# Kernel optimization log

Hardware: AMD Instinct MI355X
Metric: run time of the kernel (lower is better)

Reference implementation:

```python
import jax, jax.numpy as jnp
import numpy as np

ALPHA = 0.2  # leakyrelu negative slope
NEG_INF = -1.0e12


def setup_inputs() -> dict:
    key = jax.random.key(0)
    k1, k2, k3, k4, k5 = jax.random.split(key, 5)
    B, N, C_in, C_out = 8, 2048, 256, 256
    inp = jax.random.normal(k1, (B, N, C_in), dtype=jnp.float32)
    adj = jax.random.randint(k2, (N, N), 0, 2, dtype=jnp.int32)
    # xavier_uniform with gain=1.414 for (C_in, C_out)
    limit = 1.414 * np.sqrt(6.0 / (C_in + C_out))
    W1 = jax.random.uniform(k3, (C_in, C_out), jnp.float32, -limit, limit)
    W2 = jax.random.uniform(k4, (C_in, C_out), jnp.float32, -limit, limit)
    W3 = jax.random.uniform(k5, (C_in, C_out), jnp.float32, -limit, limit)
    return {"inp": inp, "adj": adj, "W1": W1, "W2": W2, "W3": W3}


def reference(inp, adj, W1, W2, W3):
    # inp: [B,N,Cin], adj: [N,N], W*: [Cin,Cout]
    h1 = jnp.einsum('bnc,cd->bnd', inp, W1)  # [B,N,Cout] queries
    h2 = jnp.einsum('bnc,cd->bnd', inp, W2)  # [B,N,Cout] keys
    h3 = jnp.einsum('bnc,cd->bnd', inp, W3)  # [B,N,Cout] values
    e = jnp.einsum('bnd,bmd->bnm', h1, h2)   # [B,N,N] scores
    e = jax.nn.leaky_relu(e, ALPHA)
    e = jnp.where(adj[None, :, :] > 0, e, NEG_INF)
    attention = jax.nn.softmax(e, axis=-1)   # dropout p=0 / eval mode -> identity
    h_prime = jnp.einsum('bnm,bmd->bnd', attention, h3)
    return jax.nn.relu(h_prime)  # concat=True
```

## Files before the change

### kernel.cpp

```cpp
#include <hip/hip_runtime.h>

typedef __bf16 bf16_t;
typedef __bf16 bf16x4 __attribute__((ext_vector_type(4)));
typedef __bf16 bf16x8 __attribute__((ext_vector_type(8)));
typedef float floatx4 __attribute__((ext_vector_type(4)));
typedef signed char i8_t;
typedef int intx4 __attribute__((ext_vector_type(4)));

__device__ inline void split_hl(float v, bf16_t& hi, bf16_t& lo) {
    hi = (bf16_t)v;
    lo = (bf16_t)(v - (float)hi);
}

__global__ void wtrans_kernel(const float* __restrict__ W1,
                              const float* __restrict__ W2,
                              const float* __restrict__ W3,
                              bf16_t* __restrict__ Wthi, bf16_t* __restrict__ Wtlo) {
    __shared__ float T[64 * 68];
    const int zi = blockIdx.z;
    const float* W = (zi == 0) ? W1 : ((zi == 1) ? W2 : W3);
    bf16_t* ohi = Wthi + zi * 256 * 256;
    bf16_t* olo = Wtlo + zi * 256 * 256;
    const int c0 = blockIdx.x * 64, d0 = blockIdx.y * 64;
    const int tid = threadIdx.x;
#pragma unroll
    for (int i = 0; i < 4; i++) {
        int idx = i * 256 + tid;
        int r = idx >> 4, c4 = (idx & 15) * 4;
        floatx4 v = *(const floatx4*)(W + (c0 + r) * 256 + d0 + c4);
        *(floatx4*)(&T[r * 68 + c4]) = v;
    }
    __syncthreads();
#pragma unroll
    for (int i = 0; i < 4; i++) {
        int idx = i * 256 + tid;
        int rd = idx & 63, cc4 = (idx >> 6) * 4;
        bf16x4 vh, vl;
#pragma unroll
        for (int ii = 0; ii < 4; ii++) {
            float v = T[(cc4 + ii) * 68 + rd];
            bf16_t h, l; split_hl(v, h, l);
            vh[ii] = h; vl[ii] = l;
        }
        *(bf16x4*)(ohi + (d0 + rd) * 256 + c0 + cc4) = vh;
        *(bf16x4*)(olo + (d0 + rd) * 256 + c0 + cc4) = vl;
    }
}

__global__ __launch_bounds__(256) void projadj_kernel(
    const float* __restrict__ X,
    const bf16_t* __restrict__ Wthi, const bf16_t* __restrict__ Wtlo,
    i8_t* __restrict__ Q8h, i8_t* __restrict__ Q8l, float* __restrict__ sqv,
    i8_t* __restrict__ K8h, i8_t* __restrict__ K8l, float* __restrict__ skv,
    bf16_t* __restrict__ H3t,
    const int* __restrict__ adj, unsigned* __restrict__ bits) {
    __shared__ __align__(16) char SM[51712];
    bf16_t* Xh = (bf16_t*)(SM);
    bf16_t* Xl = (bf16_t*)(SM + 5120);
    bf16_t* Wh = (bf16_t*)(SM + 10240);
    bf16_t* Wl = (bf16_t*)(SM + 30720);
    float* amS = (float*)(SM + 51200);

    const int tid = threadIdx.x;
    const int blk = blockIdx.x;
    if (blk < 512) {
        int id = blk * 256 + tid;
        const int* p = adj + (size_t)id * 32;
        unsigned wbits = 0;
#pragma unroll
        for (int j = 0; j < 32; j += 4) {
            int4 v = *(const int4*)(p + j);
            wbits |= (v.x > 0 ? 1u : 0u) << j;
            wbits |= (v.y > 0 ? 1u : 0u) << (j + 1);
            wbits |= (v.z > 0 ? 1u : 0u) << (j + 2);
            wbits |= (v.w > 0 ? 1u : 0u) << (j + 3);
        }
        bits[id] = wbits;
        return;
    }

    const int pblk = blk - 512;
    const int z = pblk >> 8;
    const int row0 = (pblk & 255) * 64;
    const int w = tid >> 6, lane = tid & 63;
    const int m = lane & 15, q = lane >> 4;
    const int wr = w >> 1, wc = w & 1;
    const bf16_t* Wzh = Wthi + z * 256 * 256;
    const bf16_t* Wzl = Wtlo + z * 256 * 256;

    floatx4 acc[16];
#pragma unroll
    for (int i = 0; i < 16; i++) acc[i] = (floatx4){0.f, 0.f, 0.f, 0.f};

    for (int c0 = 0; c0 < 256; c0 += 32) {
#pragma unroll
        for (int i = 0; i < 2; i++) {
            int idx = i * 256 + tid;
            int r = idx >> 3, c4 = (idx & 7) * 4;
            floatx4 v = *(const floatx4*)(X + (size_t)(row0 + r) * 256 + c0 + c4);
            bf16x4 vh, vl;
#pragma unroll
            for (int ii = 0; ii < 4; ii++) {
                bf16_t h, l; split_hl(v[ii], h, l);
                vh[ii] = h; vl[ii] = l;
            }
            *(bf16x4*)(&Xh[r * 40 + c4]) = vh;
            *(bf16x4*)(&Xl[r * 40 + c4]) = vl;
        }
#pragma unroll
        for (int i = 0; i < 4; i++) {
            int idx = i * 256 + tid;
            int d = idx >> 2, c8 = (idx & 3) * 8;
            *(bf16x8*)(&Wh[d * 40 + c8]) = *(const bf16x8*)(Wzh + d * 256 + c0 + c8);
            *(bf16x8*)(&Wl[d * 40 + c8]) = *(const bf16x8*)(Wzl + d * 256 + c0 + c8);
        }
        __syncthreads();
        bf16x8 ah[2], al[2];
#pragma unroll
        for (int rt = 0; rt < 2; rt++) {
            ah[rt] = *(const bf16x8*)(&Xh[(wr * 32 + rt * 16 + m) * 40 + q * 8]);
            al[rt] = *(const bf16x8*)(&Xl[(wr * 32 + rt * 16 + m) * 40 + q * 8]);
        }
#pragma unroll
        for (int ct = 0; ct < 8; ct++) {
            bf16x8 bh = *(const bf16x8*)(&Wh[(wc * 128 + ct * 16 + m) * 40 + q * 8]);
            bf16x8 bl = *(const bf16x8*)(&Wl[(wc * 128 + ct * 16 + m) * 40 + q * 8]);
#pragma unroll
            for (int rt = 0; rt < 2; rt++) {
                acc[rt * 8 + ct] = __builtin_amdgcn_mfma_f32_16x16x32_bf16(ah[rt], bh, acc[rt * 8 + ct], 0, 0, 0);
                acc[rt * 8 + ct] = __builtin_amdgcn_mfma_f32_16x16x32_bf16(ah[rt], bl, acc[rt * 8 + ct], 0, 0, 0);
                acc[rt * 8 + ct] = __builtin_amdgcn_mfma_f32_16x16x32_bf16(al[rt], bh, acc[rt * 8 + ct], 0, 0, 0);
            }
        }
        __syncthreads();
    }

    if (z < 2) {
        i8_t* Dh = (z == 0) ? Q8h : K8h;
        i8_t* Dl = (z == 0) ? Q8l : K8l;
        float* sv = (z == 0) ? sqv : skv;
        float am[2][4];
#pragma unroll
        for (int rt = 0; rt < 2; rt++)
#pragma unroll
            for (int r = 0; r < 4; r++) am[rt][r] = 0.f;
#pragma unroll
        for (int ct = 0; ct < 8; ct++)
#pragma unroll
            for (int rt = 0; rt < 2; rt++)
#pragma unroll
                for (int r = 0; r < 4; r++)
                    am[rt][r] = fmaxf(am[rt][r], fabsf(acc[rt * 8 + ct][r]));
#pragma unroll
        for (int off = 1; off < 16; off <<= 1)
#pragma unroll
            for (int rt = 0; rt < 2; rt++)
#pragma unroll
                for (int r = 0; r < 4; r++)
                    am[rt][r] = fmaxf(am[rt][r], __shfl_xor(am[rt][r], off, 64));
        if (m == 0) {
#pragma unroll
            for (int rt = 0; rt < 2; rt++)
#pragma unroll
                for (int r = 0; r < 4; r++)
                    amS[wc * 64 + wr * 32 + rt * 16 + q * 4 + r] = am[rt][r];
        }
        __syncthreads();
        float sc[2][4], inv[2][4];
#pragma unroll
        for (int rt = 0; rt < 2; rt++)
#pragma unroll
            for (int r = 0; r < 4; r++) {
                int row = wr * 32 + rt * 16 + q * 4 + r;
                float a = fmaxf(amS[row], amS[64 + row]);
                sc[rt][r]  = (a > 0.f) ? a * (1.f / 127.f) : 1.f;
                inv[rt][r] = (a > 0.f) ? 127.f / a : 0.f;
            }
#pragma unroll
        for (int ct = 0; ct < 8; ct++)
#pragma unroll
            for (int rt = 0; rt < 2; rt++)
#pragma unroll
                for (int r = 0; r < 4; r++) {
                    float vq = acc[rt * 8 + ct][r] * inv[rt][r];
                    float qh = rintf(vq);
                    float ql = fminf(fmaxf(rintf((vq - qh) * 256.f), -127.f), 127.f);
                    int offo = (row0 + wr * 32 + rt * 16 + q * 4 + r) * 256 +
                               wc * 128 + ct * 16 + m;
                    Dh[offo] = (i8_t)(int)qh;
                    Dl[offo] = (i8_t)(int)ql;
                }
        if (m == 0 && wc == 0) {
#pragma unroll
            for (int rt = 0; rt < 2; rt++)
#pragma unroll
                for (int r = 0; r < 4; r++)
                    sv[row0 + wr * 32 + rt * 16 + q * 4 + r] = sc[rt][r];
        }
    } else {
        char* VtB = SM;
#pragma unroll
        for (int ct = 0; ct < 8; ct++)
#pragma unroll
            for (int rt = 0; rt < 2; rt++) {
                int d = wc * 128 + ct * 16 + m;
                int n0 = wr * 32 + rt * 16 + q * 4;
                bf16x4 v4;
#pragma unroll
                for (int r = 0; r < 4; r++) v4[r] = (bf16_t)acc[rt * 8 + ct][r];
                *(bf16x4*)(VtB + d * 136 + n0 * 2) = v4;
            }
        __syncthreads();
        const int bb = row0 >> 11;
        const int nbase = row0 & 2047;
        bf16_t* Hrow = H3t + (size_t)bb * 256 * 2048 + nbase;
#pragma unroll
        for (int it = 0; it < 16; it++) {
            int d = it * 16 + (tid >> 4);
            int c8 = tid & 15;
            bf16x4 v = *(const bf16x4*)(VtB + d * 136 + c8 * 8);
            *(bf16x4*)(Hrow + (size_t)d * 2048 + c8 * 4) = v;
        }
    }
}

#define K8SW(row, off) ((off) ^ (((row) & 7) << 4))
#define VSW(row, off)  ((off) ^ ((((row) >> 1) & 3) << 4))
__global__ __launch_bounds__(256, 2) void attn_kernel(
    const i8_t* __restrict__ Q8h, const i8_t* __restrict__ Q8l,
    const float* __restrict__ sqv,
    const i8_t* __restrict__ K8h, const i8_t* __restrict__ K8l,
    const float* __restrict__ skv,
    const bf16_t* __restrict__ H3t, const unsigned* __restrict__ adjbits,
    bf16_t* __restrict__ Opart, float* __restrict__ mpart, float* __restrict__ lpart,
    int klen) {
    __shared__ i8_t K8[2][2][32 * 256];
    __shared__ bf16_t Vl[2][256 * 32];
    __shared__ bf16_t Pl[4][16 * 32];

    const int nwg = (int)(gridDim.x * gridDim.y * gridDim.z);
    const int wgid = (int)(blockIdx.x + (blockIdx.y << 5) + (blockIdx.z << 8));
    const int nid = (wgid & 7) * (nwg >> 3) + (wgid >> 3);
    const int qb = nid & 31;
    const int b  = (nid >> 5) & 7;
    const int kz = nid >> 8;

    const int q0 = qb * 64;
    const int tid = threadIdx.x;
    const int w = tid >> 6, lane = tid & 63;
    const int m = lane & 15, q = lane >> 4;

    char* PlB = (char*)&Pl[w][0];

    const i8_t* qrh = Q8h + (size_t)(b * 2048 + q0 + w * 16 + m) * 256;
    const i8_t* qrl = Q8l + (size_t)(b * 2048 + q0 + w * 16 + m) * 256;
    intx4 qh8[4], ql8[4];
#pragma unroll
    for (int ck = 0; ck < 4; ck++) {
        qh8[ck] = *(const intx4*)(qrh + ck * 64 + q * 16);
        ql8[ck] = *(const intx4*)(qrl + ck * 64 + q * 16);
    }
    float sq4[4];
#pragma unroll
    for (int r = 0; r < 4; r++) sq4[r] = sqv[b * 2048 + q0 + w * 16 + q * 4 + r];

    bf16x8 vones;
#pragma unroll
    for (int i = 0; i < 8; i++) vones[i] = (bf16_t)1.0f;

    float m_run[4];
#pragma unroll
    for (int r = 0; r < 4; r++) m_run[r] = -3.0e38f;
    floatx4 l_acc = (floatx4){0.f, 0.f, 0.f, 0.f};
    floatx4 o[16];
#pragma unroll
    for (int i = 0; i < 16; i++) o[i] = (floatx4){0.f, 0.f, 0.f, 0.f};

    const unsigned* bitrow[4];
#pragma unroll
    for (int r = 0; r < 4; r++)
        bitrow[r] = adjbits + (size_t)(q0 + w * 16 + q * 4 + r) * 64;

    intx4 rkh[2], rkl[2];
    bf16x8 rvv[4];
    float skt[2], skn[2];
    const int kbeg = kz * klen, kend = kbeg + klen;

#pragma unroll
    for (int i = 0; i < 2; i++) {
        int ci = i * 256 + tid;
        int kr = ci >> 4, cb = (ci & 15) * 16;
        rkh[i] = *(const intx4*)(K8h + (size_t)(b * 2048 + kbeg + kr) * 256 + cb);
        rkl[i] = *(const intx4*)(K8l + (size_t)(b * 2048 + kbeg + kr) * 256 + cb);
    }
#pragma unroll
    for (int i = 0; i < 4; i++) {
        int ci = i * 256 + tid;
        int d = ci >> 2, k8 = (ci & 3) * 8;
        rvv[i] = *(const bf16x8*)(H3t + (size_t)(b * 256 + d) * 2048 + kbeg + k8);
    }
    skt[0] = skv[b * 2048 + kbeg + m];
    skt[1] = skv[b * 2048 + kbeg + 16 + m];

    int kbuf = 0;
    for (int k0 = kbeg; k0 < kend; k0 += 32) {
        char* KB0 = (char*)&K8[kbuf][0][0];
        char* KB1 = (char*)&K8[kbuf][1][0];
        char* VB  = (char*)&Vl[kbuf][0];
#pragma unroll
        for (int i = 0; i < 2; i++) {
            int ci = i * 256 + tid;
            int kr = ci >> 4, cb = (ci & 15) * 16;
            *(intx4*)(KB0 + K8SW(kr, kr * 256 + cb)) = rkh[i];
            *(intx4*)(KB1 + K8SW(kr, kr * 256 + cb)) = rkl[i];
        }
#pragma unroll
        for (int i = 0; i < 4; i++) {
            int ci = i * 256 + tid;
            int d = ci >> 2, kb = (ci & 3) * 16;
            *(bf16x8*)(VB + VSW(d, d * 64 + kb)) = rvv[i];
        }
        __syncthreads();

        if (k0 + 32 < kend) {
            int kn = k0 + 32;
#pragma unroll
            for (int i = 0; i < 2; i++) {
                int ci = i * 256 + tid;
                int kr = ci >> 4, cb = (ci & 15) * 16;
                rkh[i] = *(const intx4*)(K8h + (size_t)(b * 2048 + kn + kr) * 256 + cb);
                rkl[i] = *(const intx4*)(K8l + (size_t)(b * 2048 + kn + kr) * 256 + cb);
            }
#pragma unroll
            for (int i = 0; i < 4; i++) {
                int ci = i * 256 + tid;
                int d = ci >> 2, k8 = (ci & 3) * 8;
                rvv[i] = *(const bf16x8*)(H3t + (size_t)(b * 256 + d) * 2048 + kn + k8);
            }
            skn[0] = skv[b * 2048 + kn + m];
            skn[1] = skv[b * 2048 + kn + 16 + m];
        }

        float s[2][4];
#pragma unroll
        for (int t = 0; t < 2; t++) {
            intx4 ch = {0, 0, 0, 0}, cm = {0, 0, 0, 0};
            const int row = t * 16 + m;
#pragma unroll
            for (int ck = 0; ck < 4; ck++) {
                const int cb2 = ck * 64 + q * 16;
                intx4 kh = *(const intx4*)(KB0 + K8SW(row, row * 256 + cb2));
                intx4 kl = *(const intx4*)(KB1 + K8SW(row, row * 256 + cb2));
                ch = __builtin_amdgcn_mfma_i32_16x16x64_i8(qh8[ck], kh, ch, 0, 0, 0);
                cm = __builtin_amdgcn_mfma_i32_16x16x64_i8(qh8[ck], kl, cm, 0, 0, 0);
                cm = __builtin_amdgcn_mfma_i32_16x16x64_i8(ql8[ck], kh, cm, 0, 0, 0);
            }
#pragma unroll
            for (int r = 0; r < 4; r++)
                s[t][r] = fmaf((float)cm[r], 0.00390625f, (float)ch[r]) * (sq4[r] * skt[t]);
        }

        unsigned aw[4];
#pragma unroll
        for (int r = 0; r < 4; r++) aw[r] = bitrow[r][k0 >> 5];
        float p[2][4], tmax[4];
#pragma unroll
        for (int r = 0; r < 4; r++) tmax[r] = -3.0e38f;
#pragma unroll
        for (int t = 0; t < 2; t++)
#pragma unroll
            for (int r = 0; r < 4; r++) {
                float v = s[t][r];
                v = (v > 0.f) ? v : 0.2f * v;
                v = ((aw[r] >> (t * 16 + m)) & 1u) ? v : -1.0e12f;
                p[t][r] = v;
                tmax[r] = fmaxf(tmax[r], v);
            }
#pragma unroll
        for (int off = 1; off < 16; off <<= 1)
#pragma unroll
            for (int r = 0; r < 4; r++)
                tmax[r] = fmaxf(tmax[r], __shfl_xor(tmax[r], off, 64));

        int rise = 0;
#pragma unroll
        for (int r = 0; r < 4; r++)
            rise |= (tmax[r] > m_run[r] + 8.f);
        if (__any(rise)) {
#pragma unroll
            for (int r = 0; r < 4; r++) {
                float mnew = fmaxf(m_run[r], tmax[r]);
                float alpha = __expf(m_run[r] - mnew);
                m_run[r] = mnew;
                l_acc[r] *= alpha;
#pragma unroll
                for (int nt = 0; nt < 16; nt++) o[nt][r] *= alpha;
            }
        }
#pragma unroll
        for (int t = 0; t < 2; t++)
#pragma unroll
            for (int r = 0; r < 4; r++)
                p[t][r] = __expf(p[t][r] - m_run[r]);

#pragma unroll
        for (int t = 0; t < 2; t++)
#pragma unroll
            for (int r = 0; r < 4; r++) {
                int row = q * 4 + r;
                *(bf16_t*)(PlB + VSW(row, row * 64 + (t * 16 + m) * 2)) = (bf16_t)p[t][r];
            }
        bf16x8 pf = *(const bf16x8*)(PlB + VSW(m, m * 64 + q * 16));

        l_acc = __builtin_amdgcn_mfma_f32_16x16x32_bf16(pf, vones, l_acc, 0, 0, 0);

#pragma unroll
        for (int nt = 0; nt < 16; nt++) {
            const int vr = nt * 16 + m;
            bf16x8 vf = *(const bf16x8*)(VB + VSW(vr, vr * 64 + q * 16));
            o[nt] = __builtin_amdgcn_mfma_f32_16x16x32_bf16(pf, vf, o[nt], 0, 0, 0);
        }
        skt[0] = skn[0];
        skt[1] = skn[1];
        kbuf ^= 1;
    }

    const int rowg = kz * 16384 + b * 2048 + q0 + w * 16 + q * 4;
#pragma unroll
    for (int nt = 0; nt < 16; nt++)
#pragma unroll
        for (int r = 0; r < 4; r++)
            Opart[(size_t)(rowg + r) * 256 + nt * 16 + m] = (bf16_t)o[nt][r];
    if (m == 0) {
#pragma unroll
        for (int r = 0; r < 4; r++) {
            mpart[rowg + r] = m_run[r];
            lpart[rowg + r] = l_acc[r];
        }
    }
}

__global__ __launch_bounds__(256) void merge_kernel(
    const bf16_t* __restrict__ Opart, const float* __restrict__ mpart,
    const float* __restrict__ lpart, float* __restrict__ out, int S) {
    int gid = blockIdx.x * 256 + threadIdx.x;
    int row = gid >> 6, c4 = (gid & 63) * 4;
    float M = -3.0e38f;
    for (int s = 0; s < S; s++) M = fmaxf(M, mpart[s * 16384 + row]);
    float denom = 0.f;
    float4 acc = make_float4(0.f, 0.f, 0.f, 0.f);
    for (int s = 0; s < S; s++) {
        float sc = __expf(mpart[s * 16384 + row] - M);
        denom += lpart[s * 16384 + row] * sc;
        bf16x4 v = *(const bf16x4*)(Opart + ((size_t)(s * 16384 + row)) * 256 + c4);
        acc.x += (float)v[0] * sc; acc.y += (float)v[1] * sc;
        acc.z += (float)v[2] * sc; acc.w += (float)v[3] * sc;
    }
    float inv = 1.f / denom;
    float4 r;
    r.x = fmaxf(acc.x * inv, 0.f);
    r.y = fmaxf(acc.y * inv, 0.f);
    r.z = fmaxf(acc.z * inv, 0.f);
    r.w = fmaxf(acc.w * inv, 0.f);
    *(float4*)(out + (size_t)row * 256 + c4) = r;
}

extern "C" void kernel_launch(void* const* d_in, const int* in_sizes, int n_in,
                              void* d_out, int out_size, void* d_ws, size_t ws_size,
                              hipStream_t stream) {
    const float* X   = (const float*)d_in[0];
    const int*   adj = (const int*)d_in[1];
    const float* W1  = (const float*)d_in[2];
    const float* W2  = (const float*)d_in[3];
    const float* W3  = (const float*)d_in[4];
    float* out = (float*)d_out;

    char* ws = (char*)d_ws;
    i8_t* Q8h = (i8_t*)(ws + ((size_t)0 << 20));
    i8_t* Q8l = (i8_t*)(ws + ((size_t)4 << 20));
    i8_t* K8h = (i8_t*)(ws + ((size_t)8 << 20));
    i8_t* K8l = (i8_t*)(ws + ((size_t)12 << 20));
    bf16_t* H3t = (bf16_t*)(ws + ((size_t)16 << 20));
    float* sqv = (float*)(ws + ((size_t)24 << 20));
    float* skv = (float*)(ws + ((size_t)24 << 20) + 65536);
    size_t wt0 = ((size_t)24 << 20) + 131072;
    bf16_t* Wthi = (bf16_t*)(ws + wt0);
    bf16_t* Wtlo = (bf16_t*)(ws + wt0 + 393216);
    float* mpart = (float*)(ws + wt0);
    float* lpart = (float*)(ws + wt0 + 131072);
    unsigned* adjb = (unsigned*)(ws + wt0 + 786432);
    size_t opart_off = wt0 + 786432 + 524288;
    const size_t need2 = opart_off + (size_t)2 * 16384 * 256 * 2;

    int S = (ws_size >= need2) ? 2 : 1;
    bf16_t* Opart = (bf16_t*)(ws + opart_off);

    wtrans_kernel<<<dim3(4, 4, 3), 256, 0, stream>>>(W1, W2, W3, Wthi, Wtlo);
    projadj_kernel<<<1280, 256, 0, stream>>>(X, Wthi, Wtlo,
                                             Q8h, Q8l, sqv, K8h, K8l, skv, H3t,
                                             adj, adjb);
    attn_kernel<<<dim3(32, 8, S), 256, 0, stream>>>(Q8h, Q8l, sqv, K8h, K8l, skv,
                                                    H3t, adjb, Opart, mpart, lpart,
                                                    2048 / S);
    merge_kernel<<<4096, 256, 0, stream>>>(Opart, mpart, lpart, out, S);
}
```

Before: 209.5 us.

## Double-buffer X tiles, read W directly from global, add MFMA priority hints

The projection kernel now register-prefetches the next X chunk and double-buffers the X shared tiles, which removes the trailing barrier per iteration. The weight fragments are no longer staged through shared memory and are loaded straight from global into registers, which shrinks the shared footprint and may raise occupancy. The attention loop wraps its MFMA sections in s_setprio to favour matrix issue across waves. The risk is that uncoalesced global weight loads per wave, relying on cache hits, could cost more than the shared-memory staging they replace.

```diff
diff --git a/kernel.cpp b/kernel.cpp
--- a/kernel.cpp
+++ b/kernel.cpp
@@ -54,12 +54,8 @@
     i8_t* __restrict__ K8h, i8_t* __restrict__ K8l, float* __restrict__ skv,
     bf16_t* __restrict__ H3t,
     const int* __restrict__ adj, unsigned* __restrict__ bits) {
-    __shared__ __align__(16) char SM[51712];
-    bf16_t* Xh = (bf16_t*)(SM);
-    bf16_t* Xl = (bf16_t*)(SM + 5120);
-    bf16_t* Wh = (bf16_t*)(SM + 10240);
-    bf16_t* Wl = (bf16_t*)(SM + 30720);
-    float* amS = (float*)(SM + 51200);
+    __shared__ __align__(16) char SM[34816];
+    float* amS = (float*)(SM + 20480);
 
     const int tid = threadIdx.x;
     const int blk = blockIdx.x;
@@ -85,36 +81,42 @@
     const int w = tid >> 6, lane = tid & 63;
     const int m = lane & 15, q = lane >> 4;
     const int wr = w >> 1, wc = w & 1;
-    const bf16_t* Wzh = Wthi + z * 256 * 256;
-    const bf16_t* Wzl = Wtlo + z * 256 * 256;
+
+    const bf16_t* wbh = Wthi + (size_t)z * 256 * 256 + (wc * 128 + m) * 256 + q * 8;
+    const bf16_t* wbl = Wtlo + (size_t)z * 256 * 256 + (wc * 128 + m) * 256 + q * 8;
+
+    const int xr_r[2] = { (0 * 256 + tid) >> 3, (1 * 256 + tid) >> 3 };
+    const int xr_c4 = (tid & 7) * 4;
+    floatx4 xr[2];
+#pragma unroll
+    for (int i = 0; i < 2; i++)
+        xr[i] = *(const floatx4*)(X + (size_t)(row0 + xr_r[i]) * 256 + 0 + xr_c4);
 
     floatx4 acc[16];
 #pragma unroll
     for (int i = 0; i < 16; i++) acc[i] = (floatx4){0.f, 0.f, 0.f, 0.f};
 
-    for (int c0 = 0; c0 < 256; c0 += 32) {
+    int buf = 0;
+    for (int c0 = 0; c0 < 256; c0 += 32, buf ^= 1) {
+        bf16_t* Xh = (bf16_t*)(SM + buf * 10240);
+        bf16_t* Xl = Xh + 2560;
 #pragma unroll
         for (int i = 0; i < 2; i++) {
-            int idx = i * 256 + tid;
-            int r = idx >> 3, c4 = (idx & 7) * 4;
-            floatx4 v = *(const floatx4*)(X + (size_t)(row0 + r) * 256 + c0 + c4);
             bf16x4 vh, vl;
 #pragma unroll
             for (int ii = 0; ii < 4; ii++) {
-                bf16_t h, l; split_hl(v[ii], h, l);
+                bf16_t h, l; split_hl(xr[i][ii], h, l);
                 vh[ii] = h; vl[ii] = l;
             }
-            *(bf16x4*)(&Xh[r * 40 + c4]) = vh;
-            *(bf16x4*)(&Xl[r * 40 + c4]) = vl;
-        }
-#pragma unroll
-        for (int i = 0; i < 4; i++) {
-            int idx = i * 256 + tid;
-            int d = idx >> 2, c8 = (idx & 3) * 8;
-            *(bf16x8*)(&Wh[d * 40 + c8]) = *(const bf16x8*)(Wzh + d * 256 + c0 + c8);
-            *(bf16x8*)(&Wl[d * 40 + c8]) = *(const bf16x8*)(Wzl + d * 256 + c0 + c8);
+            *(bf16x4*)(&Xh[xr_r[i] * 40 + xr_c4]) = vh;
+            *(bf16x4*)(&Xl[xr_r[i] * 40 + xr_c4]) = vl;
         }
         __syncthreads();
+        if (c0 + 32 < 256) {
+#pragma unroll
+            for (int i = 0; i < 2; i++)
+                xr[i] = *(const floatx4*)(X + (size_t)(row0 + xr_r[i]) * 256 + c0 + 32 + xr_c4);
+        }
         bf16x8 ah[2], al[2];
 #pragma unroll
         for (int rt = 0; rt < 2; rt++) {
@@ -123,8 +125,8 @@
         }
 #pragma unroll
         for (int ct = 0; ct < 8; ct++) {
-            bf16x8 bh = *(const bf16x8*)(&Wh[(wc * 128 + ct * 16 + m) * 40 + q * 8]);
-            bf16x8 bl = *(const bf16x8*)(&Wl[(wc * 128 + ct * 16 + m) * 40 + q * 8]);
+            bf16x8 bh = *(const bf16x8*)(wbh + (size_t)(ct * 16) * 256 + c0);
+            bf16x8 bl = *(const bf16x8*)(wbl + (size_t)(ct * 16) * 256 + c0);
 #pragma unroll
             for (int rt = 0; rt < 2; rt++) {
                 acc[rt * 8 + ct] = __builtin_amdgcn_mfma_f32_16x16x32_bf16(ah[rt], bh, acc[rt * 8 + ct], 0, 0, 0);
@@ -132,7 +134,6 @@
                 acc[rt * 8 + ct] = __builtin_amdgcn_mfma_f32_16x16x32_bf16(al[rt], bh, acc[rt * 8 + ct], 0, 0, 0);
             }
         }
-        __syncthreads();
     }
 
     if (z < 2) {
@@ -198,6 +199,7 @@
                     sv[row0 + wr * 32 + rt * 16 + q * 4 + r] = sc[rt][r];
         }
     } else {
+        __syncthreads();
         char* VtB = SM;
 #pragma unroll
         for (int ct = 0; ct < 8; ct++)
@@ -342,6 +344,7 @@
         }
 
         float s[2][4];
+        __builtin_amdgcn_s_setprio(1);
 #pragma unroll
         for (int t = 0; t < 2; t++) {
             intx4 ch = {0, 0, 0, 0}, cm = {0, 0, 0, 0};
@@ -359,6 +362,7 @@
             for (int r = 0; r < 4; r++)
                 s[t][r] = fmaf((float)cm[r], 0.00390625f, (float)ch[r]) * (sq4[r] * skt[t]);
         }
+        __builtin_amdgcn_s_setprio(0);
 
         unsigned aw[4];
 #pragma unroll
@@ -412,14 +416,15 @@
             }
         bf16x8 pf = *(const bf16x8*)(PlB + VSW(m, m * 64 + q * 16));
 
+        __builtin_amdgcn_s_setprio(1);
         l_acc = __builtin_amdgcn_mfma_f32_16x16x32_bf16(pf, vones, l_acc, 0, 0, 0);
-
 #pragma unroll
         for (int nt = 0; nt < 16; nt++) {
             const int vr = nt * 16 + m;
             bf16x8 vf = *(const bf16x8*)(VB + VSW(vr, vr * 64 + q * 16));
             o[nt] = __builtin_amdgcn_mfma_f32_16x16x32_bf16(pf, vf, o[nt], 0, 0, 0);
         }
+        __builtin_amdgcn_s_setprio(0);
         skt[0] = skn[0];
         skt[1] = skn[1];
         kbuf ^= 1;
```

Measured after the change: 222.6 us. 6.3% more time.
